# Performance work log

Measured on AMD Instinct MI355X. Metric: run time of the kernel, lower is better.

The kernel has to match this reference:

```python
import jax, jax.numpy as jnp
import numpy as np

N = 50000      # nodes
E = 800000     # edges (avg degree 16)
D_IN = 128
D_H = 128
D_OUT = 64
L = 3          # num_layers
NEG_SLOPE = 0.1


def setup_inputs() -> dict:
    key = jax.random.key(0)
    ks = jax.random.split(key, 8)
    s = 0.05
    return {
        "x": jax.random.normal(ks[0], (N, D_IN), jnp.float32),
        "edge_index": jax.random.randint(ks[1], (2, E), 0, N),
        # SAGEConv params per layer: lin_l (neighbors, with bias), lin_r (root)
        "wl": jax.random.normal(ks[2], (L, D_H, D_H), jnp.float32) * s,
        "wr": jax.random.normal(ks[3], (L, D_H, D_H), jnp.float32) * s,
        "bc": jnp.zeros((L, D_H), jnp.float32),
        # per-layer Linear params (first L-1 are hidden->hidden)
        "wlin": jax.random.normal(ks[4], (L - 1, D_H, D_H), jnp.float32) * s,
        "blin": jnp.zeros((L - 1, D_H), jnp.float32),
        # final Linear hidden->out
        "wout": jax.random.normal(ks[5], (D_H, D_OUT), jnp.float32) * s,
        "bout": jnp.zeros((D_OUT,), jnp.float32),
    }


def _sage_conv(x, src, dst, wl, wr, b):
    # mean aggregation of source features at destination nodes
    n = x.shape[0]
    agg = jax.ops.segment_sum(x[src], dst, num_segments=n)        # [N, d]
    cnt = jax.ops.segment_sum(jnp.ones((src.shape[0],), x.dtype), dst, num_segments=n)
    agg = agg / jnp.maximum(cnt, 1.0)[:, None]
    return agg @ wl + x @ wr + b


def _lrelu(v):
    return jnp.where(v > 0, v, NEG_SLOPE * v)


def reference(x, edge_index, wl, wr, bc, wlin, blin, wout, bout):
    src, dst = edge_index[0], edge_index[1]
    for i in range(L - 1):
        x = _lrelu(_sage_conv(x, src, dst, wl[i], wr[i], bc[i]))
        x = _lrelu(x @ wlin[i] + blin[i])
    x = _sage_conv(x, src, dst, wl[L - 1], wr[L - 1], bc[L - 1])
    return x @ wout + bout
```

## Files before the change

### kernel.cpp

```cpp
#include <hip/hip_runtime.h>

#define NEG_SLOPE 0.1f

typedef __bf16 bf16x8 __attribute__((ext_vector_type(8)));
typedef float f32x4 __attribute__((ext_vector_type(4)));
typedef unsigned int uint32x4 __attribute__((ext_vector_type(4)));
typedef unsigned short ushort;

__device__ inline ushort f2bf(float f) {
    unsigned int u = __float_as_uint(f);
    u += 0x7fffu + ((u >> 16) & 1u);
    return (ushort)(u >> 16);
}
__device__ inline float bf2f(ushort h) { return __uint_as_float(((unsigned int)h) << 16); }

__device__ inline void pack8(const float* v, uint32x4& hv, uint32x4& lv) {
    ushort hi[8], lo[8];
#pragma unroll
    for (int j = 0; j < 8; j++) {
        float f = v[j];
        ushort h = f2bf(f);
        hi[j] = h;
        lo[j] = f2bf(f - bf2f(h));
    }
    hv.x = hi[0] | ((unsigned)hi[1] << 16); hv.y = hi[2] | ((unsigned)hi[3] << 16);
    hv.z = hi[4] | ((unsigned)hi[5] << 16); hv.w = hi[6] | ((unsigned)hi[7] << 16);
    lv.x = lo[0] | ((unsigned)lo[1] << 16); lv.y = lo[2] | ((unsigned)lo[3] << 16);
    lv.z = lo[4] | ((unsigned)lo[5] << 16); lv.w = lo[6] | ((unsigned)lo[7] << 16);
}

__global__ void k_count(const int* __restrict__ ei, int E, int* __restrict__ degp,
                        int* __restrict__ rank) {
    int e = blockIdx.x * 256 + threadIdx.x;
    if (e < E) rank[e] = atomicAdd(&degp[(size_t)ei[E + e] * 16], 1);
}

__global__ void k_starts(const int* __restrict__ degp, int N, int* __restrict__ start,
                         int* __restrict__ deg, int* __restrict__ counter) {
    int n = blockIdx.x * 256 + threadIdx.x;
    int lane = threadIdx.x & 63;
    int d = (n < N) ? degp[(size_t)n * 16] : 0;
    int inc = d;
#pragma unroll
    for (int o = 1; o < 64; o <<= 1) {
        int v = __shfl_up(inc, o);
        if (lane >= o) inc += v;
    }
    int total = __shfl(inc, 63);
    int base = 0;
    if (lane == 0) base = atomicAdd(counter, total);
    base = __shfl(base, 0);
    int st = base + inc - d;
    if (n < N) { start[n] = st; deg[n] = d; }
}

__global__ void k_fill(const int* __restrict__ ei, int E, const int* __restrict__ start,
                       const int* __restrict__ rank, int* __restrict__ adj) {
    int e = blockIdx.x * 256 + threadIdx.x;
    if (e < E) {
        int s = ei[e];
        int dv = ei[E + e];
        adj[start[dv] + rank[e]] = s;
    }
}


__global__ __launch_bounds__(256) void k_wpack(const float* __restrict__ wl,
                                               const float* __restrict__ wr,
                                               const float* __restrict__ wlin,
                                               const float* __restrict__ wout,
                                               ushort* __restrict__ wph,
                                               ushort* __restrict__ wpl) {
    int m = blockIdx.y;
    int c = blockIdx.x * 256 + threadIdx.x;
    const float* src;
    int Nn = 128;
    size_t dstoff;
    if (m < 3)      { src = wl   + (size_t)m * 16384;       dstoff = (size_t)m * 16384; }
    else if (m < 6) { src = wr   + (size_t)(m - 3) * 16384; dstoff = (size_t)m * 16384; }
    else if (m < 8) { src = wlin + (size_t)(m - 6) * 16384; dstoff = (size_t)m * 16384; }
    else            { src = wout; Nn = 64;                  dstoff = (size_t)8 * 16384; }
    if (c >= Nn * 16) return;
    int cb = c >> 8, gg = (c >> 4) & 15, col = c & 15;
    float v[8];
#pragma unroll
    for (int j = 0; j < 8; j++)
        v[j] = src[(size_t)(gg * 8 + j) * Nn + cb * 16 + col];
    uint32x4 hv, lv;
    pack8(v, hv, lv);
    *(uint32x4*)(wph + dstoff + (size_t)c * 8) = hv;
    *(uint32x4*)(wpl + dstoff + (size_t)c * 8) = lv;
}


__global__ __launch_bounds__(256) void k_splitx(const float* __restrict__ x,
                                                ushort* __restrict__ oh,
                                                ushort* __restrict__ ol, int N) {
    int t = blockIdx.x * 256 + threadIdx.x;
    int row = t >> 4, g = t & 15;
    if (row >= N) return;
    const float* src = x + (size_t)row * 128 + g * 8;
    float v[8];
#pragma unroll
    for (int j = 0; j < 8; j++) v[j] = src[j];
    uint32x4 hv, lv;
    pack8(v, hv, lv);
    size_t off = (size_t)row * 128 + g * 8;
    *(uint32x4*)(oh + off) = hv;
    *(uint32x4*)(ol + off) = lv;
}


__global__ __launch_bounds__(256) void k_agg(const ushort* __restrict__ xh,
                                             const int* __restrict__ adj,
                                             const int* __restrict__ start,
                                             const int* __restrict__ deg,
                                             ushort* __restrict__ oh,
                                             ushort* __restrict__ ol, int N) {
    int node = (blockIdx.x * 256 + threadIdx.x) >> 4;
    if (node >= N) return;
    const int q = threadIdx.x & 15;
    const int st = start[node], cnt = deg[node];
    float a0 = 0, a1 = 0, a2 = 0, a3 = 0, a4 = 0, a5 = 0, a6 = 0, a7 = 0;
    int i = 0;
    for (; i + 4 <= cnt; i += 4) {
        int s0 = adj[st + i], s1 = adj[st + i + 1], s2 = adj[st + i + 2], s3 = adj[st + i + 3];
        uint32x4 u0 = *(const uint32x4*)(xh + (size_t)s0 * 128 + q * 8);
        uint32x4 u1 = *(const uint32x4*)(xh + (size_t)s1 * 128 + q * 8);
        uint32x4 u2 = *(const uint32x4*)(xh + (size_t)s2 * 128 + q * 8);
        uint32x4 u3 = *(const uint32x4*)(xh + (size_t)s3 * 128 + q * 8);
#pragma unroll
        for (int e = 0; e < 4; e++) {
            uint32x4 u = e == 0 ? u0 : e == 1 ? u1 : e == 2 ? u2 : u3;
            a0 += __uint_as_float(u.x << 16); a1 += __uint_as_float(u.x & 0xffff0000u);
            a2 += __uint_as_float(u.y << 16); a3 += __uint_as_float(u.y & 0xffff0000u);
            a4 += __uint_as_float(u.z << 16); a5 += __uint_as_float(u.z & 0xffff0000u);
            a6 += __uint_as_float(u.w << 16); a7 += __uint_as_float(u.w & 0xffff0000u);
        }
    }
    for (; i < cnt; i++) {
        int s0 = adj[st + i];
        uint32x4 u = *(const uint32x4*)(xh + (size_t)s0 * 128 + q * 8);
        a0 += __uint_as_float(u.x << 16); a1 += __uint_as_float(u.x & 0xffff0000u);
        a2 += __uint_as_float(u.y << 16); a3 += __uint_as_float(u.y & 0xffff0000u);
        a4 += __uint_as_float(u.z << 16); a5 += __uint_as_float(u.z & 0xffff0000u);
        a6 += __uint_as_float(u.w << 16); a7 += __uint_as_float(u.w & 0xffff0000u);
    }
    float inv = 1.0f / fmaxf((float)cnt, 1.0f);
    float v[8] = {a0 * inv, a1 * inv, a2 * inv, a3 * inv,
                  a4 * inv, a5 * inv, a6 * inv, a7 * inv};
    uint32x4 hv, lv;
    pack8(v, hv, lv);
    size_t off = (size_t)node * 128 + q * 8;
    *(uint32x4*)(oh + off) = hv;
    *(uint32x4*)(ol + off) = lv;
}


template <bool ACT1, int NM2, bool ACT2, bool FINAL>
__global__ __launch_bounds__(256) void k_layer(
    const ushort* __restrict__ aggh, const ushort* __restrict__ aggl,
    const ushort* __restrict__ hh,   const ushort* __restrict__ hl,
    const ushort* __restrict__ w1h,  const ushort* __restrict__ w1l,
    const ushort* __restrict__ w2h,  const ushort* __restrict__ w2l,
    const float* __restrict__ b1,
    const ushort* __restrict__ w3h,  const ushort* __restrict__ w3l,
    const float* __restrict__ b2,
    ushort* __restrict__ oh, ushort* __restrict__ ol,
    float* __restrict__ of, int N) {
    constexpr int NCF2 = NM2 / 64;
    __shared__ ushort th[64][136];
    __shared__ ushort tl[64][136];

    const int tid = threadIdx.x;
    const int w = tid >> 6, lane = tid & 63;
    const int g = lane >> 4, r16 = lane & 15;
    const int m0 = blockIdx.x * 64;

    size_t ro[4];
#pragma unroll
    for (int rf = 0; rf < 4; rf++) {
        int row = m0 + rf * 16 + r16;
        if (row > N - 1) row = N - 1;
        ro[rf] = (size_t)row * 128 + g * 8;
    }

    f32x4 acc[4][2];
#pragma unroll
    for (int rf = 0; rf < 4; rf++)
#pragma unroll
        for (int cf = 0; cf < 2; cf++) acc[rf][cf] = (f32x4){0.f, 0.f, 0.f, 0.f};

#pragma unroll
    for (int s = 0; s < 4; s++) {
        bf16x8 a1h_[4], a1l_[4], a2h_[4], a2l_[4];
#pragma unroll
        for (int rf = 0; rf < 4; rf++) {
            size_t o = ro[rf] + s * 32;
            a1h_[rf] = *(const bf16x8*)(aggh + o);
            a1l_[rf] = *(const bf16x8*)(aggl + o);
            a2h_[rf] = *(const bf16x8*)(hh + o);
            a2l_[rf] = *(const bf16x8*)(hl + o);
        }
        bf16x8 b1h_[2], b1l_[2], b2h_[2], b2l_[2];
#pragma unroll
        for (int cf = 0; cf < 2; cf++) {
            size_t o = (size_t)(w * 2 + cf) * 2048 + s * 512 + g * 128 + r16 * 8;
            b1h_[cf] = *(const bf16x8*)(w1h + o);
            b1l_[cf] = *(const bf16x8*)(w1l + o);
            b2h_[cf] = *(const bf16x8*)(w2h + o);
            b2l_[cf] = *(const bf16x8*)(w2l + o);
        }
#pragma unroll
        for (int rf = 0; rf < 4; rf++)
#pragma unroll
            for (int cf = 0; cf < 2; cf++) {
                acc[rf][cf] = __builtin_amdgcn_mfma_f32_16x16x32_bf16(a1h_[rf], b1h_[cf], acc[rf][cf], 0, 0, 0);
                acc[rf][cf] = __builtin_amdgcn_mfma_f32_16x16x32_bf16(a1h_[rf], b1l_[cf], acc[rf][cf], 0, 0, 0);
                acc[rf][cf] = __builtin_amdgcn_mfma_f32_16x16x32_bf16(a1l_[rf], b1h_[cf], acc[rf][cf], 0, 0, 0);
                acc[rf][cf] = __builtin_amdgcn_mfma_f32_16x16x32_bf16(a2h_[rf], b2h_[cf], acc[rf][cf], 0, 0, 0);
                acc[rf][cf] = __builtin_amdgcn_mfma_f32_16x16x32_bf16(a2h_[rf], b2l_[cf], acc[rf][cf], 0, 0, 0);
                acc[rf][cf] = __builtin_amdgcn_mfma_f32_16x16x32_bf16(a2l_[rf], b2h_[cf], acc[rf][cf], 0, 0, 0);
            }
    }

    {
        float bv1[2];
#pragma unroll
        for (int cf = 0; cf < 2; cf++) bv1[cf] = b1[(w * 2 + cf) * 16 + r16];
#pragma unroll
        for (int rf = 0; rf < 4; rf++)
#pragma unroll
            for (int cf = 0; cf < 2; cf++)
#pragma unroll
                for (int i = 0; i < 4; i++) {
                    float v = acc[rf][cf][i] + bv1[cf];
                    if (ACT1) v = v > 0.f ? v : NEG_SLOPE * v;
                    ushort hi = f2bf(v);
                    ushort lo = f2bf(v - bf2f(hi));
                    th[rf * 16 + g * 4 + i][w * 32 + cf * 16 + r16] = hi;
                    tl[rf * 16 + g * 4 + i][w * 32 + cf * 16 + r16] = lo;
                }
    }
    __syncthreads();

    f32x4 acc2[4][NCF2];
#pragma unroll
    for (int rf = 0; rf < 4; rf++)
#pragma unroll
        for (int cf = 0; cf < NCF2; cf++) acc2[rf][cf] = (f32x4){0.f, 0.f, 0.f, 0.f};

#pragma unroll
    for (int s = 0; s < 4; s++) {
        bf16x8 ah_[4], al_[4];
#pragma unroll
        for (int rf = 0; rf < 4; rf++) {
            ah_[rf] = *(const bf16x8*)&th[rf * 16 + r16][s * 32 + g * 8];
            al_[rf] = *(const bf16x8*)&tl[rf * 16 + r16][s * 32 + g * 8];
        }
        bf16x8 wh_[NCF2], wlo_[NCF2];
#pragma unroll
        for (int cf = 0; cf < NCF2; cf++) {
            size_t o = (size_t)(w * NCF2 + cf) * 2048 + s * 512 + g * 128 + r16 * 8;
            wh_[cf] = *(const bf16x8*)(w3h + o);
            wlo_[cf] = *(const bf16x8*)(w3l + o);
        }
#pragma unroll
        for (int rf = 0; rf < 4; rf++)
#pragma unroll
            for (int cf = 0; cf < NCF2; cf++) {
                acc2[rf][cf] = __builtin_amdgcn_mfma_f32_16x16x32_bf16(ah_[rf], wh_[cf], acc2[rf][cf], 0, 0, 0);
                acc2[rf][cf] = __builtin_amdgcn_mfma_f32_16x16x32_bf16(ah_[rf], wlo_[cf], acc2[rf][cf], 0, 0, 0);
                acc2[rf][cf] = __builtin_amdgcn_mfma_f32_16x16x32_bf16(al_[rf], wh_[cf], acc2[rf][cf], 0, 0, 0);
            }
    }

    if constexpr (FINAL) {
        float bv2 = b2[w * 16 + r16];
#pragma unroll
        for (int rf = 0; rf < 4; rf++)
#pragma unroll
            for (int i = 0; i < 4; i++) {
                int row = m0 + rf * 16 + g * 4 + i;
                if (row < N) of[(size_t)row * 64 + w * 16 + r16] = acc2[rf][0][i] + bv2;
            }
    } else {
        __syncthreads();
        float bv2[2];
#pragma unroll
        for (int cf = 0; cf < 2; cf++) bv2[cf] = b2[(w * 2 + cf) * 16 + r16];
#pragma unroll
        for (int rf = 0; rf < 4; rf++)
#pragma unroll
            for (int cf = 0; cf < 2; cf++)
#pragma unroll
                for (int i = 0; i < 4; i++) {
                    float v = acc2[rf][cf][i] + bv2[cf];
                    if (ACT2) v = v > 0.f ? v : NEG_SLOPE * v;
                    ushort hi = f2bf(v);
                    ushort lo = f2bf(v - bf2f(hi));
                    th[rf * 16 + g * 4 + i][w * 32 + cf * 16 + r16] = hi;
                    tl[rf * 16 + g * 4 + i][w * 32 + cf * 16 + r16] = lo;
                }
        __syncthreads();
#pragma unroll
        for (int rep = 0; rep < 4; rep++) {
            int id = rep * 256 + tid;
            int row = id >> 4, kg = id & 15;
            int grow = m0 + row;
            if (grow < N) {
                uint32x4 hv = *(const uint32x4*)&th[row][kg * 8];
                uint32x4 lv = *(const uint32x4*)&tl[row][kg * 8];
                *(uint32x4*)(oh + (size_t)grow * 128 + kg * 8) = hv;
                *(uint32x4*)(ol + (size_t)grow * 128 + kg * 8) = lv;
            }
        }
    }
}


extern "C" void kernel_launch(void* const* d_in, const int* in_sizes, int n_in,
                              void* d_out, int out_size, void* d_ws, size_t ws_size,
                              hipStream_t stream) {
    const float* x    = (const float*)d_in[0];
    const int*   ei   = (const int*)d_in[1];
    const float* wl   = (const float*)d_in[2];
    const float* wr   = (const float*)d_in[3];
    const float* bc   = (const float*)d_in[4];
    const float* wlin = (const float*)d_in[5];
    const float* blin = (const float*)d_in[6];
    const float* wout = (const float*)d_in[7];
    const float* bout = (const float*)d_in[8];
    float* out = (float*)d_out;

    const int N = in_sizes[0] / 128;
    const int E = in_sizes[1] / 2;

    char* p = (char*)d_ws;
    auto alloc = [&](size_t bytes) {
        char* r = p;
        p += (bytes + 255) & ~(size_t)255;
        return r;
    };
    int* counter = (int*)alloc(4);
    int* degp    = (int*)alloc((size_t)N * 16 * 4);
    int* deg     = (int*)alloc((size_t)N * 4);
    int* start   = (int*)alloc((size_t)N * 4);
    int* rank    = (int*)alloc((size_t)E * 4);
    int* adj     = (int*)alloc((size_t)E * 4);
    ushort* wph  = (ushort*)alloc((size_t)139264 * 2);
    ushort* wpl  = (ushort*)alloc((size_t)139264 * 2);
    ushort* xh   = (ushort*)alloc((size_t)N * 128 * 2);
    ushort* xl   = (ushort*)alloc((size_t)N * 128 * 2);
    ushort* aggh = (ushort*)alloc((size_t)N * 128 * 2);
    ushort* aggl = (ushort*)alloc((size_t)N * 128 * 2);
    ushort* hAh  = (ushort*)alloc((size_t)N * 128 * 2);
    ushort* hAl  = (ushort*)alloc((size_t)N * 128 * 2);

    hipMemsetAsync(d_ws, 0, (size_t)((char*)(degp + (size_t)N * 16) - (char*)d_ws), stream);

    const int gE = (E + 255) / 256;
    const int gN = (N + 255) / 256;
    const int gQ = (N * 16 + 255) / 256;
    const int gB = (N + 63) / 64;

    k_count <<<gE, 256, 0, stream>>>(ei, E, degp, rank);
    k_starts<<<gN, 256, 0, stream>>>(degp, N, start, deg, counter);
    k_fill  <<<gE, 256, 0, stream>>>(ei, E, start, rank, adj);
    k_wpack <<<dim3(8, 9), 256, 0, stream>>>(wl, wr, wlin, wout, wph, wpl);
    k_splitx<<<gQ, 256, 0, stream>>>(x, xh, xl, N);

    const ushort *wl0h = wph,           *wl0l = wpl;
    const ushort *wl1h = wph + 16384,   *wl1l = wpl + 16384;
    const ushort *wl2h = wph + 32768,   *wl2l = wpl + 32768;
    const ushort *wr0h = wph + 3*16384, *wr0l = wpl + 3*16384;
    const ushort *wr1h = wph + 4*16384, *wr1l = wpl + 4*16384;
    const ushort *wr2h = wph + 5*16384, *wr2l = wpl + 5*16384;
    const ushort *wn0h = wph + 6*16384, *wn0l = wpl + 6*16384;
    const ushort *wn1h = wph + 7*16384, *wn1l = wpl + 7*16384;
    const ushort *woh  = wph + 8*16384, *wol  = wpl + 8*16384;

    k_agg<<<gQ, 256, 0, stream>>>(xh, adj, start, deg, aggh, aggl, N);
    k_layer<true, 128, true, false><<<gB, 256, 0, stream>>>(
        aggh, aggl, xh, xl, wl0h, wl0l, wr0h, wr0l, bc,
        wn0h, wn0l, blin, hAh, hAl, nullptr, N);
    k_agg<<<gQ, 256, 0, stream>>>(hAh, adj, start, deg, aggh, aggl, N);
    k_layer<true, 128, true, false><<<gB, 256, 0, stream>>>(
        aggh, aggl, hAh, hAl, wl1h, wl1l, wr1h, wr1l, bc + 128,
        wn1h, wn1l, blin + 128, xh, xl, nullptr, N);
    k_agg<<<gQ, 256, 0, stream>>>(xh, adj, start, deg, aggh, aggl, N);
    k_layer<false, 64, false, true><<<gB, 256, 0, stream>>>(
        aggh, aggl, xh, xl, wl2h, wl2l, wr2h, wr2l, bc + 256,
        woh, wol, bout, nullptr, nullptr, out, N);
}
```

Measured before the change: 364.8 us.

## Fuse neighbor mean aggregation into per-layer GEMM kernel via shared memory

Removes the separate aggregation kernel and computes each block's 32 aggregated rows directly into LDS, then feeds them to the MFMA GEMMs from shared memory. This eliminates writing and re-reading the N×128 hi/lo aggregate buffers and three kernel launches. Block tile shrinks from 64 to 32 rows to keep the gather parallelism, which halves weight reuse per block and doubles the number of blocks reading weights. An extra barrier is added before the LDS tile is reused for the hidden activations.

Measured after the change: 323.0 us. 1.13x faster.

```diff
diff --git a/kernel.cpp b/kernel.cpp
--- a/kernel.cpp
+++ b/kernel.cpp
@@ -111,56 +111,11 @@
 }
 
 
-__global__ __launch_bounds__(256) void k_agg(const ushort* __restrict__ xh,
-                                             const int* __restrict__ adj,
-                                             const int* __restrict__ start,
-                                             const int* __restrict__ deg,
-                                             ushort* __restrict__ oh,
-                                             ushort* __restrict__ ol, int N) {
-    int node = (blockIdx.x * 256 + threadIdx.x) >> 4;
-    if (node >= N) return;
-    const int q = threadIdx.x & 15;
-    const int st = start[node], cnt = deg[node];
-    float a0 = 0, a1 = 0, a2 = 0, a3 = 0, a4 = 0, a5 = 0, a6 = 0, a7 = 0;
-    int i = 0;
-    for (; i + 4 <= cnt; i += 4) {
-        int s0 = adj[st + i], s1 = adj[st + i + 1], s2 = adj[st + i + 2], s3 = adj[st + i + 3];
-        uint32x4 u0 = *(const uint32x4*)(xh + (size_t)s0 * 128 + q * 8);
-        uint32x4 u1 = *(const uint32x4*)(xh + (size_t)s1 * 128 + q * 8);
-        uint32x4 u2 = *(const uint32x4*)(xh + (size_t)s2 * 128 + q * 8);
-        uint32x4 u3 = *(const uint32x4*)(xh + (size_t)s3 * 128 + q * 8);
-#pragma unroll
-        for (int e = 0; e < 4; e++) {
-            uint32x4 u = e == 0 ? u0 : e == 1 ? u1 : e == 2 ? u2 : u3;
-            a0 += __uint_as_float(u.x << 16); a1 += __uint_as_float(u.x & 0xffff0000u);
-            a2 += __uint_as_float(u.y << 16); a3 += __uint_as_float(u.y & 0xffff0000u);
-            a4 += __uint_as_float(u.z << 16); a5 += __uint_as_float(u.z & 0xffff0000u);
-            a6 += __uint_as_float(u.w << 16); a7 += __uint_as_float(u.w & 0xffff0000u);
-        }
-    }
-    for (; i < cnt; i++) {
-        int s0 = adj[st + i];
-        uint32x4 u = *(const uint32x4*)(xh + (size_t)s0 * 128 + q * 8);
-        a0 += __uint_as_float(u.x << 16); a1 += __uint_as_float(u.x & 0xffff0000u);
-        a2 += __uint_as_float(u.y << 16); a3 += __uint_as_float(u.y & 0xffff0000u);
-        a4 += __uint_as_float(u.z << 16); a5 += __uint_as_float(u.z & 0xffff0000u);
-        a6 += __uint_as_float(u.w << 16); a7 += __uint_as_float(u.w & 0xffff0000u);
-    }
-    float inv = 1.0f / fmaxf((float)cnt, 1.0f);
-    float v[8] = {a0 * inv, a1 * inv, a2 * inv, a3 * inv,
-                  a4 * inv, a5 * inv, a6 * inv, a7 * inv};
-    uint32x4 hv, lv;
-    pack8(v, hv, lv);
-    size_t off = (size_t)node * 128 + q * 8;
-    *(uint32x4*)(oh + off) = hv;
-    *(uint32x4*)(ol + off) = lv;
-}
-
-
 template <bool ACT1, int NM2, bool ACT2, bool FINAL>
-__global__ __launch_bounds__(256) void k_layer(
-    const ushort* __restrict__ aggh, const ushort* __restrict__ aggl,
+__global__ __launch_bounds__(256) void k_fused(
     const ushort* __restrict__ hh,   const ushort* __restrict__ hl,
+    const int* __restrict__ adj, const int* __restrict__ start,
+    const int* __restrict__ deg,
     const ushort* __restrict__ w1h,  const ushort* __restrict__ w1l,
     const ushort* __restrict__ w2h,  const ushort* __restrict__ w2l,
     const float* __restrict__ b1,
@@ -169,38 +124,83 @@
     ushort* __restrict__ oh, ushort* __restrict__ ol,
     float* __restrict__ of, int N) {
     constexpr int NCF2 = NM2 / 64;
-    __shared__ ushort th[64][136];
-    __shared__ ushort tl[64][136];
+    __shared__ ushort th[32][136];
+    __shared__ ushort tl[32][136];
 
     const int tid = threadIdx.x;
     const int w = tid >> 6, lane = tid & 63;
     const int g = lane >> 4, r16 = lane & 15;
-    const int m0 = blockIdx.x * 64;
-
-    size_t ro[4];
-#pragma unroll
-    for (int rf = 0; rf < 4; rf++) {
+    const int m0 = blockIdx.x * 32;
+
+    {
+        const int qw = tid >> 4;
+        const int q = tid & 15;
+#pragma unroll
+        for (int rep = 0; rep < 2; rep++) {
+            int nr = qw + rep * 16;
+            int node = m0 + nr;
+            if (node > N - 1) node = N - 1;
+            int st = start[node], cnt = deg[node];
+            float a0 = 0, a1 = 0, a2 = 0, a3 = 0, a4 = 0, a5 = 0, a6 = 0, a7 = 0;
+            int i = 0;
+            for (; i + 4 <= cnt; i += 4) {
+                int s0 = adj[st + i], s1 = adj[st + i + 1];
+                int s2 = adj[st + i + 2], s3 = adj[st + i + 3];
+                uint32x4 u0 = *(const uint32x4*)(hh + (size_t)s0 * 128 + q * 8);
+                uint32x4 u1 = *(const uint32x4*)(hh + (size_t)s1 * 128 + q * 8);
+                uint32x4 u2 = *(const uint32x4*)(hh + (size_t)s2 * 128 + q * 8);
+                uint32x4 u3 = *(const uint32x4*)(hh + (size_t)s3 * 128 + q * 8);
+#pragma unroll
+                for (int e = 0; e < 4; e++) {
+                    uint32x4 u = e == 0 ? u0 : e == 1 ? u1 : e == 2 ? u2 : u3;
+                    a0 += __uint_as_float(u.x << 16); a1 += __uint_as_float(u.x & 0xffff0000u);
+                    a2 += __uint_as_float(u.y << 16); a3 += __uint_as_float(u.y & 0xffff0000u);
+                    a4 += __uint_as_float(u.z << 16); a5 += __uint_as_float(u.z & 0xffff0000u);
+                    a6 += __uint_as_float(u.w << 16); a7 += __uint_as_float(u.w & 0xffff0000u);
+                }
+            }
+            for (; i < cnt; i++) {
+                int s0 = adj[st + i];
+                uint32x4 u = *(const uint32x4*)(hh + (size_t)s0 * 128 + q * 8);
+                a0 += __uint_as_float(u.x << 16); a1 += __uint_as_float(u.x & 0xffff0000u);
+                a2 += __uint_as_float(u.y << 16); a3 += __uint_as_float(u.y & 0xffff0000u);
+                a4 += __uint_as_float(u.z << 16); a5 += __uint_as_float(u.z & 0xffff0000u);
+                a6 += __uint_as_float(u.w << 16); a7 += __uint_as_float(u.w & 0xffff0000u);
+            }
+            float inv = 1.0f / fmaxf((float)cnt, 1.0f);
+            float v[8] = {a0 * inv, a1 * inv, a2 * inv, a3 * inv,
+                          a4 * inv, a5 * inv, a6 * inv, a7 * inv};
+            uint32x4 hv, lv;
+            pack8(v, hv, lv);
+            *(uint32x4*)&th[nr][q * 8] = hv;
+            *(uint32x4*)&tl[nr][q * 8] = lv;
+        }
+    }
+    __syncthreads();
+
+    size_t ro[2];
+#pragma unroll
+    for (int rf = 0; rf < 2; rf++) {
         int row = m0 + rf * 16 + r16;
         if (row > N - 1) row = N - 1;
         ro[rf] = (size_t)row * 128 + g * 8;
     }
 
-    f32x4 acc[4][2];
-#pragma unroll
-    for (int rf = 0; rf < 4; rf++)
+    f32x4 acc[2][2];
+#pragma unroll
+    for (int rf = 0; rf < 2; rf++)
 #pragma unroll
         for (int cf = 0; cf < 2; cf++) acc[rf][cf] = (f32x4){0.f, 0.f, 0.f, 0.f};
 
 #pragma unroll
     for (int s = 0; s < 4; s++) {
-        bf16x8 a1h_[4], a1l_[4], a2h_[4], a2l_[4];
-#pragma unroll
-        for (int rf = 0; rf < 4; rf++) {
-            size_t o = ro[rf] + s * 32;
-            a1h_[rf] = *(const bf16x8*)(aggh + o);
-            a1l_[rf] = *(const bf16x8*)(aggl + o);
-            a2h_[rf] = *(const bf16x8*)(hh + o);
-            a2l_[rf] = *(const bf16x8*)(hl + o);
+        bf16x8 a1h_[2], a1l_[2], a2h_[2], a2l_[2];
+#pragma unroll
+        for (int rf = 0; rf < 2; rf++) {
+            a1h_[rf] = *(const bf16x8*)&th[rf * 16 + r16][s * 32 + g * 8];
+            a1l_[rf] = *(const bf16x8*)&tl[rf * 16 + r16][s * 32 + g * 8];
+            a2h_[rf] = *(const bf16x8*)(hh + ro[rf] + s * 32);
+            a2l_[rf] = *(const bf16x8*)(hl + ro[rf] + s * 32);
         }
         bf16x8 b1h_[2], b1l_[2], b2h_[2], b2l_[2];
 #pragma unroll
@@ -212,7 +212,7 @@
             b2l_[cf] = *(const bf16x8*)(w2l + o);
         }
 #pragma unroll
-        for (int rf = 0; rf < 4; rf++)
+        for (int rf = 0; rf < 2; rf++)
 #pragma unroll
             for (int cf = 0; cf < 2; cf++) {
                 acc[rf][cf] = __builtin_amdgcn_mfma_f32_16x16x32_bf16(a1h_[rf], b1h_[cf], acc[rf][cf], 0, 0, 0);
@@ -223,13 +223,14 @@
                 acc[rf][cf] = __builtin_amdgcn_mfma_f32_16x16x32_bf16(a2l_[rf], b2h_[cf], acc[rf][cf], 0, 0, 0);
             }
     }
+    __syncthreads();
 
     {
         float bv1[2];
 #pragma unroll
         for (int cf = 0; cf < 2; cf++) bv1[cf] = b1[(w * 2 + cf) * 16 + r16];
 #pragma unroll
-        for (int rf = 0; rf < 4; rf++)
+        for (int rf = 0; rf < 2; rf++)
 #pragma unroll
             for (int cf = 0; cf < 2; cf++)
 #pragma unroll
@@ -244,17 +245,17 @@
     }
     __syncthreads();
 
-    f32x4 acc2[4][NCF2];
-#pragma unroll
-    for (int rf = 0; rf < 4; rf++)
+    f32x4 acc2[2][NCF2];
+#pragma unroll
+    for (int rf = 0; rf < 2; rf++)
 #pragma unroll
         for (int cf = 0; cf < NCF2; cf++) acc2[rf][cf] = (f32x4){0.f, 0.f, 0.f, 0.f};
 
 #pragma unroll
     for (int s = 0; s < 4; s++) {
-        bf16x8 ah_[4], al_[4];
-#pragma unroll
-        for (int rf = 0; rf < 4; rf++) {
+        bf16x8 ah_[2], al_[2];
+#pragma unroll
+        for (int rf = 0; rf < 2; rf++) {
             ah_[rf] = *(const bf16x8*)&th[rf * 16 + r16][s * 32 + g * 8];
             al_[rf] = *(const bf16x8*)&tl[rf * 16 + r16][s * 32 + g * 8];
         }
@@ -266,7 +267,7 @@
             wlo_[cf] = *(const bf16x8*)(w3l + o);
         }
 #pragma unroll
-        for (int rf = 0; rf < 4; rf++)
+        for (int rf = 0; rf < 2; rf++)
 #pragma unroll
             for (int cf = 0; cf < NCF2; cf++) {
                 acc2[rf][cf] = __builtin_amdgcn_mfma_f32_16x16x32_bf16(ah_[rf], wh_[cf], acc2[rf][cf], 0, 0, 0);
@@ -278,7 +279,7 @@
     if constexpr (FINAL) {
         float bv2 = b2[w * 16 + r16];
 #pragma unroll
-        for (int rf = 0; rf < 4; rf++)
+        for (int rf = 0; rf < 2; rf++)
 #pragma unroll
             for (int i = 0; i < 4; i++) {
                 int row = m0 + rf * 16 + g * 4 + i;
@@ -290,7 +291,7 @@
 #pragma unroll
         for (int cf = 0; cf < 2; cf++) bv2[cf] = b2[(w * 2 + cf) * 16 + r16];
 #pragma unroll
-        for (int rf = 0; rf < 4; rf++)
+        for (int rf = 0; rf < 2; rf++)
 #pragma unroll
             for (int cf = 0; cf < 2; cf++)
 #pragma unroll
@@ -304,7 +305,7 @@
                 }
         __syncthreads();
 #pragma unroll
-        for (int rep = 0; rep < 4; rep++) {
+        for (int rep = 0; rep < 2; rep++) {
             int id = rep * 256 + tid;
             int row = id >> 4, kg = id & 15;
             int grow = m0 + row;
@@ -352,8 +353,6 @@
     ushort* wpl  = (ushort*)alloc((size_t)139264 * 2);
     ushort* xh   = (ushort*)alloc((size_t)N * 128 * 2);
     ushort* xl   = (ushort*)alloc((size_t)N * 128 * 2);
-    ushort* aggh = (ushort*)alloc((size_t)N * 128 * 2);
-    ushort* aggl = (ushort*)alloc((size_t)N * 128 * 2);
     ushort* hAh  = (ushort*)alloc((size_t)N * 128 * 2);
     ushort* hAl  = (ushort*)alloc((size_t)N * 128 * 2);
 
@@ -362,7 +361,7 @@
     const int gE = (E + 255) / 256;
     const int gN = (N + 255) / 256;
     const int gQ = (N * 16 + 255) / 256;
-    const int gB = (N + 63) / 64;
+    const int gF = (N + 31) / 32;
 
     k_count <<<gE, 256, 0, stream>>>(ei, E, degp, rank);
     k_starts<<<gN, 256, 0, stream>>>(degp, N, start, deg, counter);
@@ -380,16 +379,13 @@
     const ushort *wn1h = wph + 7*16384, *wn1l = wpl + 7*16384;
     const ushort *woh  = wph + 8*16384, *wol  = wpl + 8*16384;
 
-    k_agg<<<gQ, 256, 0, stream>>>(xh, adj, start, deg, aggh, aggl, N);
-    k_layer<true, 128, true, false><<<gB, 256, 0, stream>>>(
-        aggh, aggl, xh, xl, wl0h, wl0l, wr0h, wr0l, bc,
+    k_fused<true, 128, true, false><<<gF, 256, 0, stream>>>(
+        xh, xl, adj, start, deg, wl0h, wl0l, wr0h, wr0l, bc,
         wn0h, wn0l, blin, hAh, hAl, nullptr, N);
-    k_agg<<<gQ, 256, 0, stream>>>(hAh, adj, start, deg, aggh, aggl, N);
-    k_layer<true, 128, true, false><<<gB, 256, 0, stream>>>(
-        aggh, aggl, hAh, hAl, wl1h, wl1l, wr1h, wr1l, bc + 128,
+    k_fused<true, 128, true, false><<<gF, 256, 0, stream>>>(
+        hAh, hAl, adj, start, deg, wl1h, wl1l, wr1h, wr1l, bc + 128,
         wn1h, wn1l, blin + 128, xh, xl, nullptr, N);
-    k_agg<<<gQ, 256, 0, stream>>>(xh, adj, start, deg, aggh, aggl, N);
-    k_layer<false, 64, false, true><<<gB, 256, 0, stream>>>(
-        aggh, aggl, xh, xl, wl2h, wl2l, wr2h, wr2l, bc + 256,
+    k_fused<false, 64, false, true><<<gF, 256, 0, stream>>>(
+        xh, xl, adj, start, deg, wl2h, wl2l, wr2h, wr2l, bc + 256,
         woh, wol, bout, nullptr, nullptr, out, N);
 }
```
